# Performance work log

Hardware: AMD Instinct MI355X
Metric: run time of the kernel (lower is better)

The kernel has to match this reference:

```python
import jax, jax.numpy as jnp
import numpy as np

N_GAUSSIANS = 16
B, D = 32768, 64
LOG_2PI = float(np.log(2.0 * np.pi))


def setup_inputs() -> dict:
    key = jax.random.key(0)
    k1, k2, k3, k4 = jax.random.split(key, 4)
    means = jax.random.normal(k1, (B, N_GAUSSIANS * D), dtype=jnp.float32)
    # strictly positive diagonal variances in [0.5, 1.5)
    covs = jax.random.uniform(k2, (B, N_GAUSSIANS * D), dtype=jnp.float32) + 0.5
    # positive mixture weights (softmax-normalized, like a typical MDN head)
    weights = jax.nn.softmax(jax.random.normal(k3, (B, N_GAUSSIANS), dtype=jnp.float32), axis=-1)
    targets = jax.random.normal(k4, (B, D), dtype=jnp.float32)
    return {"means": means, "covs": covs, "weights": weights, "targets": targets}


def reference(means, covs, weights, targets):
    b = means.shape[0]
    mu = means.reshape(b, N_GAUSSIANS, -1)   # [B, K, D]
    var = covs.reshape(b, N_GAUSSIANS, -1)   # [B, K, D]
    t = targets[:, None, :]                  # [B, 1, D]
    d = mu.shape[-1]
    # analytic diagonal-Gaussian log-prob (same math as MultivariateNormal
    # with diag_embed covariance, without the Cholesky)
    quad = jnp.sum((t - mu) ** 2 / var, axis=-1)          # [B, K]
    logdet = jnp.sum(jnp.log(var), axis=-1)               # [B, K]
    log_probs = -0.5 * (d * LOG_2PI + logdet + quad)      # [B, K]
    log_probs = jnp.clip(log_probs, -100.0, 0.0)
    log_probs_weighted = log_probs + jnp.log(weights)
    total_log_likelihood = jax.nn.logsumexp(log_probs_weighted, axis=1)  # [B]
    return -1.0 * total_log_likelihood
```

## Files before the change

### kernel.cpp

```cpp
#include <hip/hip_runtime.h>
#include <math.h>

#define NG 16
#define DIM 64
#define LOG_2PI 1.8378770664093453f

__global__ __launch_bounds__(256) void gmm_loss_kernel(
    const float* __restrict__ means,
    const float* __restrict__ covs,
    const float* __restrict__ weights,
    const float* __restrict__ targets,
    float* __restrict__ out)
{
    const int b = blockIdx.x;
    const int tid = threadIdx.x;
    const int lane = tid & 63;

    __shared__ float sbuf[NG];

    const float4* m4 = (const float4*)(means + (size_t)b * (NG * DIM));
    const float4* v4 = (const float4*)(covs  + (size_t)b * (NG * DIM));
    const float4* t4 = (const float4*)(targets + (size_t)b * DIM);

    const float4 m = m4[tid];
    const float4 v = v4[tid];
    const float4 t = t4[tid & 15];

    float dx = t.x - m.x;
    float p  = dx * dx * __builtin_amdgcn_rcpf(v.x);
    dx = t.y - m.y;
    p += dx * dx * __builtin_amdgcn_rcpf(v.y);
    dx = t.z - m.z;
    p += dx * dx * __builtin_amdgcn_rcpf(v.z);
    dx = t.w - m.w;
    p += dx * dx * __builtin_amdgcn_rcpf(v.w);
    p += __logf(v.x * v.y * v.z * v.w);

    p += __shfl_xor(p, 1);
    p += __shfl_xor(p, 2);
    p += __shfl_xor(p, 4);
    p += __shfl_xor(p, 8);

    if ((lane & 15) == 0) sbuf[tid >> 4] = p;
    __syncthreads();

    if (tid < 64) {
        const int g = lane & 15;
        const float s = sbuf[g];
        float lp = -0.5f * (DIM * LOG_2PI + s);
        lp = fminf(fmaxf(lp, -100.0f), 0.0f);
        const float lw = lp + __logf(weights[(size_t)b * NG + g]);

        float M = lw;
        M = fmaxf(M, __shfl_xor(M, 1));
        M = fmaxf(M, __shfl_xor(M, 2));
        M = fmaxf(M, __shfl_xor(M, 4));
        M = fmaxf(M, __shfl_xor(M, 8));
        float e = __expf(lw - M);
        e += __shfl_xor(e, 1);
        e += __shfl_xor(e, 2);
        e += __shfl_xor(e, 4);
        e += __shfl_xor(e, 8);

        if (tid == 0) out[b] = -(M + __logf(e));
    }
}

extern "C" void kernel_launch(void* const* d_in, const int* in_sizes, int n_in,
                              void* d_out, int out_size, void* d_ws, size_t ws_size,
                              hipStream_t stream) {
    const float* means   = (const float*)d_in[0];
    const float* covs    = (const float*)d_in[1];
    const float* weights = (const float*)d_in[2];
    const float* targets = (const float*)d_in[3];
    float* out = (float*)d_out;

    const int B = in_sizes[0] / (NG * DIM);
    gmm_loss_kernel<<<B, 256, 0, stream>>>(means, covs, weights, targets, out);
}
```

Before: 275.5 us.

## Map one mixture row per wavefront and loop rows, removing block-level sync

```diff
diff --git a/kernel.cpp b/kernel.cpp
--- a/kernel.cpp
+++ b/kernel.cpp
@@ -4,65 +4,83 @@
 #define NG 16
 #define DIM 64
 #define LOG_2PI 1.8378770664093453f
+#define RPW 4
+#define WPB 4
+#define ROWS_PER_BLOCK (RPW * WPB)
 
 __global__ __launch_bounds__(256) void gmm_loss_kernel(
     const float* __restrict__ means,
     const float* __restrict__ covs,
     const float* __restrict__ weights,
     const float* __restrict__ targets,
-    float* __restrict__ out)
+    float* __restrict__ out, int B)
 {
-    const int b = blockIdx.x;
-    const int tid = threadIdx.x;
-    const int lane = tid & 63;
+    const int lane = threadIdx.x & 63;
+    const int wave = threadIdx.x >> 6;
+    const int g  = lane >> 2;
+    const int dq = lane & 3;
+    const int fo = lane * 4;
 
-    __shared__ float sbuf[NG];
+    int b = blockIdx.x * ROWS_PER_BLOCK + wave * RPW;
 
-    const float4* m4 = (const float4*)(means + (size_t)b * (NG * DIM));
-    const float4* v4 = (const float4*)(covs  + (size_t)b * (NG * DIM));
-    const float4* t4 = (const float4*)(targets + (size_t)b * DIM);
+    #pragma unroll 1
+    for (int r = 0; r < RPW; ++r, ++b) {
+        if (b >= B) break;
 
-    const float4 m = m4[tid];
-    const float4 v = v4[tid];
-    const float4 t = t4[tid & 15];
+        const float4* m4 = (const float4*)(means + (size_t)b * (NG * DIM)) + fo;
+        const float4* v4 = (const float4*)(covs  + (size_t)b * (NG * DIM)) + fo;
+        const float4* t4 = (const float4*)(targets + (size_t)b * DIM) + dq * 4;
 
-    float dx = t.x - m.x;
-    float p  = dx * dx * __builtin_amdgcn_rcpf(v.x);
-    dx = t.y - m.y;
-    p += dx * dx * __builtin_amdgcn_rcpf(v.y);
-    dx = t.z - m.z;
-    p += dx * dx * __builtin_amdgcn_rcpf(v.z);
-    dx = t.w - m.w;
-    p += dx * dx * __builtin_amdgcn_rcpf(v.w);
-    p += __logf(v.x * v.y * v.z * v.w);
+        const float  w  = weights[(size_t)b * NG + g];
+        const float4 m0 = m4[0], m1 = m4[1], m2 = m4[2], m3 = m4[3];
+        const float4 v0 = v4[0], v1 = v4[1], v2 = v4[2], v3 = v4[3];
+        const float4 t0 = t4[0], t1 = t4[1], t2 = t4[2], t3 = t4[3];
 
-    p += __shfl_xor(p, 1);
-    p += __shfl_xor(p, 2);
-    p += __shfl_xor(p, 4);
-    p += __shfl_xor(p, 8);
+        float p = 0.0f;
+        float dx;
+        dx = t0.x - m0.x; p += dx * dx * __builtin_amdgcn_rcpf(v0.x);
+        dx = t0.y - m0.y; p += dx * dx * __builtin_amdgcn_rcpf(v0.y);
+        dx = t0.z - m0.z; p += dx * dx * __builtin_amdgcn_rcpf(v0.z);
+        dx = t0.w - m0.w; p += dx * dx * __builtin_amdgcn_rcpf(v0.w);
+        p += __logf(v0.x * v0.y * v0.z * v0.w);
 
-    if ((lane & 15) == 0) sbuf[tid >> 4] = p;
-    __syncthreads();
+        dx = t1.x - m1.x; p += dx * dx * __builtin_amdgcn_rcpf(v1.x);
+        dx = t1.y - m1.y; p += dx * dx * __builtin_amdgcn_rcpf(v1.y);
+        dx = t1.z - m1.z; p += dx * dx * __builtin_amdgcn_rcpf(v1.z);
+        dx = t1.w - m1.w; p += dx * dx * __builtin_amdgcn_rcpf(v1.w);
+        p += __logf(v1.x * v1.y * v1.z * v1.w);
 
-    if (tid < 64) {
-        const int g = lane & 15;
-        const float s = sbuf[g];
-        float lp = -0.5f * (DIM * LOG_2PI + s);
+        dx = t2.x - m2.x; p += dx * dx * __builtin_amdgcn_rcpf(v2.x);
+        dx = t2.y - m2.y; p += dx * dx * __builtin_amdgcn_rcpf(v2.y);
+        dx = t2.z - m2.z; p += dx * dx * __builtin_amdgcn_rcpf(v2.z);
+        dx = t2.w - m2.w; p += dx * dx * __builtin_amdgcn_rcpf(v2.w);
+        p += __logf(v2.x * v2.y * v2.z * v2.w);
+
+        dx = t3.x - m3.x; p += dx * dx * __builtin_amdgcn_rcpf(v3.x);
+        dx = t3.y - m3.y; p += dx * dx * __builtin_amdgcn_rcpf(v3.y);
+        dx = t3.z - m3.z; p += dx * dx * __builtin_amdgcn_rcpf(v3.z);
+        dx = t3.w - m3.w; p += dx * dx * __builtin_amdgcn_rcpf(v3.w);
+        p += __logf(v3.x * v3.y * v3.z * v3.w);
+
+        p += __shfl_xor(p, 1);
+        p += __shfl_xor(p, 2);
+
+        float lp = -0.5f * (DIM * LOG_2PI + p);
         lp = fminf(fmaxf(lp, -100.0f), 0.0f);
-        const float lw = lp + __logf(weights[(size_t)b * NG + g]);
+        const float lw = lp + __logf(w);
 
         float M = lw;
-        M = fmaxf(M, __shfl_xor(M, 1));
-        M = fmaxf(M, __shfl_xor(M, 2));
         M = fmaxf(M, __shfl_xor(M, 4));
         M = fmaxf(M, __shfl_xor(M, 8));
+        M = fmaxf(M, __shfl_xor(M, 16));
+        M = fmaxf(M, __shfl_xor(M, 32));
         float e = __expf(lw - M);
-        e += __shfl_xor(e, 1);
-        e += __shfl_xor(e, 2);
         e += __shfl_xor(e, 4);
         e += __shfl_xor(e, 8);
+        e += __shfl_xor(e, 16);
+        e += __shfl_xor(e, 32);
 
-        if (tid == 0) out[b] = -(M + __logf(e));
+        if (lane == 0) out[b] = -(M + __logf(e));
     }
 }
 
@@ -76,5 +94,6 @@
     float* out = (float*)d_out;
 
     const int B = in_sizes[0] / (NG * DIM);
-    gmm_loss_kernel<<<B, 256, 0, stream>>>(means, covs, weights, targets, out);
+    const int grid = (B + ROWS_PER_BLOCK - 1) / ROWS_PER_BLOCK;
+    gmm_loss_kernel<<<grid, 256, 0, stream>>>(means, covs, weights, targets, out, B);
 }
```

Result: no change. 280.0 us (+1.6%).
